# Kernel tuning notes

Measured on AMD Instinct MI355X. Metric: run time of the kernel, lower is better.

Reference implementation:

```python
import jax, jax.numpy as jnp
import numpy as np

R = 4                      # search_range
D = 2 * R + 1              # 9 -> 81 cost channels
FILTERS = [128, 128, 96, 64, 32, 2]


def mish(x):
    return x * jnp.tanh(jax.nn.softplus(x))


def sep_conv(x, dw, pw, b, act):
    # depthwise 3x3 (depth_multiplier=1), then pointwise 1x1, bias after pointwise
    y = jax.lax.conv_general_dilated(
        x, dw, window_strides=(1, 1), padding='SAME',
        dimension_numbers=('NHWC', 'HWIO', 'NHWC'),
        feature_group_count=x.shape[-1])
    y = jax.lax.conv_general_dilated(
        y, pw, window_strides=(1, 1), padding='SAME',
        dimension_numbers=('NHWC', 'HWIO', 'NHWC'))
    if b is not None:
        y = y + b
    return mish(y) if act else y


def cost_volume(prv, nxt):
    B, H, W, C = prv.shape
    pad = jnp.pad(nxt, ((0, 0), (R, R), (R, R), (0, 0)))
    # (2R+1)^2 shifted correlations, mean over channels (matches tf.reduce_mean axis=3)
    costs = [jnp.mean(prv * pad[:, i:i + H, j:j + W, :], axis=3)
             for i in range(D) for j in range(D)]
    return jnp.stack(costs, axis=3)  # [B,H,W,81]


def setup_inputs() -> dict:
    key = jax.random.key(0)
    ks = jax.random.split(key, 40)
    B, H, W, C = 8, 128, 128, 128
    inp = {
        'prv': jax.random.normal(ks[0], (B, H, W, C), jnp.float32),
        'nxt': jax.random.normal(ks[1], (B, H, W, C), jnp.float32),
    }
    in_ch = [D * D + 2 * C] + FILTERS[:-1]  # [337,128,128,96,64,32]
    ki = 2
    for i, (ci, f) in enumerate(zip(in_ch, FILTERS)):
        inp[f'dw{i}'] = jax.random.normal(ks[ki], (3, 3, 1, ci), jnp.float32) * 0.05; ki += 1
        inp[f'pw{i}'] = jax.random.normal(ks[ki], (1, 1, ci, f), jnp.float32) * 0.05; ki += 1
        if i < len(FILTERS) - 1:  # last layer: use_bias=False
            inp[f'b{i}'] = jnp.zeros((f,), jnp.float32)
    return inp


def reference(prv, nxt,
              dw0, pw0, b0, dw1, pw1, b1, dw2, pw2, b2,
              dw3, pw3, b3, dw4, pw4, b4, dw5, pw5):
    cost = cost_volume(prv, nxt)
    x = jnp.concatenate([cost, prv, nxt], axis=-1)
    x = sep_conv(x, dw0, pw0, b0, True)
    x = sep_conv(x, dw1, pw1, b1, True)
    x = sep_conv(x, dw2, pw2, b2, True)
    x = sep_conv(x, dw3, pw3, b3, True)
    x = sep_conv(x, dw4, pw4, b4, True)
    x = sep_conv(x, dw5, pw5, None, False)  # flow head: no bias, no activation
    return x
```

## Files before the change

kernel.cpp:

```cpp
#include <hip/hip_runtime.h>
#include <math.h>

#define BATCH 8
#define HH 128
#define WW 128
#define CC 128
#define RR 4
#define DDIM 9
#define NS 81
#define NSP 96
#define HWPIX (HH*WW)
#define DSLAB 1032

typedef short  short8  __attribute__((ext_vector_type(8)));
typedef float  f32x4   __attribute__((ext_vector_type(4)));

__device__ __forceinline__ short bf16h(float f){
    unsigned u = __float_as_uint(f);
    u += 0x7fffu + ((u >> 16) & 1u);
    return (short)(u >> 16);
}
__device__ __forceinline__ float bf16f(short s){
    return __uint_as_float(((unsigned)(unsigned short)s) << 16);
}
__device__ __forceinline__ float mish_f(float x){
    float xc = fminf(x, 30.f);
    float t = expf(xc);
    float u = t*t + 2.f*t;
    return x * (u / (u + 2.f));
}

__device__ __forceinline__ void gld16(float* lds, const float* g){
    __builtin_amdgcn_global_load_lds(
        (const __attribute__((address_space(1))) unsigned int*)g,
        (__attribute__((address_space(3))) unsigned int*)lds, 16, 0, 0);
}

__device__ __forceinline__ void lds_barrier(){
    __asm volatile("s_waitcnt lgkmcnt(0)\n\ts_barrier" ::: "memory");
}

__global__ void zero_k(float* p, int n){
    int i = blockIdx.x*256 + threadIdx.x;
    if(i < n) p[i] = 0.f;
}

__global__ __launch_bounds__(256,2) void cost_kernel(
    const float* __restrict__ prv, const float* __restrict__ nxt,
    const float* __restrict__ zb, float* __restrict__ cost)
{
    __shared__ float nx[2][576*12];
    const int tid = threadIdx.x;
    const int tx = tid & 15, ty = tid >> 4;
    const int x0 = blockIdx.x*16, y0 = blockIdx.y*16, b = blockIdx.z;

    float acc[NS];
#pragma unroll
    for(int s=0;s<NS;s++) acc[s]=0.f;

    const float* prvp = prv + (((size_t)b*HH + (y0+ty))*WW + (x0+tx))*CC;
    const float* nxb  = nxt + (size_t)b*HH*WW*CC;

    auto stagec = [&](int c0, int pb){
        float* xp = &nx[pb][0];
#pragma unroll
        for(int it=0;it<7;it++){
            int e = it*256 + tid;
            if(e < 1728){
                int px = e/3, q = e - px*3;
                int hy = y0 - RR + px/24, hx = x0 - RR + px%24;
                bool ok = (q < 2) && hy>=0 && hy<HH && hx>=0 && hx<WW;
                const float* gp = ok ? (nxb + ((size_t)hy*WW + hx)*CC + c0 + q*4)
                                     : zb;
                gld16(xp + px*12 + q*4, gp);
            }
        }
    };

    float4 pAr = *(const float4*)(prvp);
    float4 pBr = *(const float4*)(prvp + 4);
    stagec(0, 0);
    int pb = 0;
    for(int c0=0;c0<CC;c0+=8){
        __syncthreads();
        float4 A = pAr, Bv = pBr;
        if(c0+8 < CC){
            pAr = *(const float4*)(prvp + c0 + 8);
            pBr = *(const float4*)(prvp + c0 + 12);
            stagec(c0+8, pb^1);
        }
        const float* xp = &nx[pb][0];
#pragma unroll
        for(int i=0;i<DDIM;i++){
#pragma unroll
            for(int j=0;j<DDIM;j++){
                const float* q = &xp[((ty+i)*24 + (tx+j))*12];
                float4 n0 = *(const float4*)q;
                float4 n1 = *(const float4*)(q+4);
                float s = acc[i*DDIM+j];
                s = fmaf(A.x,n0.x,s);  s = fmaf(A.y,n0.y,s);
                s = fmaf(A.z,n0.z,s);  s = fmaf(A.w,n0.w,s);
                s = fmaf(Bv.x,n1.x,s); s = fmaf(Bv.y,n1.y,s);
                s = fmaf(Bv.z,n1.z,s); s = fmaf(Bv.w,n1.w,s);
                acc[i*DDIM+j] = s;
            }
        }
        pb ^= 1;
    }
    float* op = cost + (((size_t)b*HH + (y0+ty))*WW + (x0+tx))*NSP;
#pragma unroll
    for(int g=0; g<NSP/4; g++){
        float4 v;
        int s = g*4;
        v.x = (s   < NS) ? acc[s  ]*(1.f/128.f) : 0.f;
        v.y = (s+1 < NS) ? acc[s+1]*(1.f/128.f) : 0.f;
        v.z = (s+2 < NS) ? acc[s+2]*(1.f/128.f) : 0.f;
        v.w = (s+3 < NS) ? acc[s+3]*(1.f/128.f) : 0.f;
        *(float4*)(op + s) = v;
    }
}

__global__ void prep_pw(const float* __restrict__ src, short* __restrict__ dh,
                        short* __restrict__ dl, int K, int N, int NP, int total,
                        int remap)
{
    int idx = blockIdx.x*256 + threadIdx.x;
    if(idx >= total) return;
    int j  = idx & 7;
    int n  = (idx>>3) % NP;
    int k8 = (idx>>3) / NP;
    int k  = k8*8 + j;
    if(remap) k = (k < 81) ? k : ((k < 96) ? -1 : k - 15);
    float v = (k>=0 && k<K && n<N) ? src[(size_t)k*N + n] : 0.f;
    short h = bf16h(v);
    dh[idx] = h;
    dl[idx] = bf16h(v - bf16f(h));
}

__global__ void prep_dw(const float* __restrict__ src, float* __restrict__ dst,
                        int K, int K0, int remap, int total)
{
    int idx = blockIdx.x*256 + threadIdx.x;
    if(idx >= total) return;
    int k = idx / K0, c = idx - k*K0;
    int cr = c;
    if(remap) cr = (c < 81) ? c : ((c < 96) ? -1 : c - 15);
    dst[idx] = (cr>=0 && cr<K) ? src[k*K + cr] : 0.f;
}

template<int CINR,int K0,int COUT,int NP,bool BIAS,bool ACT,bool CONCAT>
__global__ __launch_bounds__(256,2) void sep_mfma(
    const float* __restrict__ xin, const float* __restrict__ cost,
    const float* __restrict__ prv, const float* __restrict__ nxt,
    const float* __restrict__ dwp, const short* __restrict__ wh,
    const short* __restrict__ wl, const float* __restrict__ bias,
    const float* __restrict__ zb, float* __restrict__ out)
{
    constexpr int TN = NP/32;
    __shared__ float xs[2][180*36];
    __shared__ short dshh[4*DSLAB];
    __shared__ short dshl[4*DSLAB];
    __shared__ float dwls[2][9*32];

    const int tid = threadIdx.x;
    const int x0 = blockIdx.x*16, y0 = blockIdx.y*8, b = blockIdx.z;
    const int lane = tid & 63;
    const int wv   = tid >> 6;
    const int wm   = wv >> 1, wn = wv & 1;
    const int l15  = lane & 15, quad = lane >> 4;

    f32x4 acc[4][TN];
#pragma unroll
    for(int i=0;i<4;i++)
#pragma unroll
        for(int nt=0;nt<TN;nt++) acc[i][nt] = (f32x4){0.f,0.f,0.f,0.f};

    auto stage = [&](int c0, int pb){
        if(tid < 72)
            gld16(&dwls[pb][(tid>>3)*32 + (tid&7)*4],
                  dwp + (tid>>3)*K0 + c0 + (tid&7)*4);
        const float* src; int str, coff;
        if(CONCAT){
            if(c0 < 96)      { src = cost; str = NSP; coff = c0; }
            else if(c0 < 224){ src = prv;  str = 128; coff = c0-96; }
            else             { src = nxt;  str = 128; coff = c0-224; }
        } else { src = xin; str = CINR; coff = c0; }
        const float* sb = src + (size_t)b*HH*WW*str + coff;
        float* xp = &xs[pb][0];
#pragma unroll
        for(int it=0;it<7;it++){
            int e = it*256 + tid;
            if(e < 1620){
                int hp = e/9, q = e - hp*9;
                int hy = y0-1 + hp/18, hx = x0-1 + hp%18;
                bool ok = (q < 8) && hy>=0 && hy<HH && hx>=0 && hx<WW;
                const float* gp = ok ? (sb + ((size_t)hy*WW + hx)*str + q*4)
                                     : zb;
                gld16(xp + hp*36 + q*4, gp);
            }
        }
    };

    const int c4  = tid & 7;
    const int pxg = tid >> 3;
    const int dpy = pxg >> 2;
    const int dxb = (pxg & 3) * 4;

    stage(0, 0);
    int pb = 0;
    for(int c0=0;c0<K0;c0+=32){
        __syncthreads();
        const int k8 = (c0>>3) + quad;
        short8 Bh[TN], Bl[TN];
#pragma unroll
        for(int nt=0;nt<TN;nt++){
            int n = wn*(NP/2) + nt*16 + l15;
            size_t off = ((size_t)k8*NP + n)*8;
            Bh[nt] = *(const short8*)(wh + off);
            Bl[nt] = *(const short8*)(wl + off);
        }
        if(c0+32 < K0) stage(c0+32, pb^1);
        const float* xp = &xs[pb][0];
        const float* dwc = &dwls[pb][0];
        {
            float4 o[4];
#pragma unroll
            for(int dx=0;dx<4;dx++) o[dx] = make_float4(0.f,0.f,0.f,0.f);
#pragma unroll
            for(int kh=0;kh<3;kh++){
                float4 xw[6];
#pragma unroll
                for(int t=0;t<6;t++)
                    xw[t] = *(const float4*)&xp[((dpy+kh)*18 + dxb + t)*36 + c4*4];
#pragma unroll
                for(int kw=0;kw<3;kw++){
                    float4 w4 = *(const float4*)&dwc[(kh*3+kw)*32 + c4*4];
#pragma unroll
                    for(int dx=0;dx<4;dx++){
                        float4 xv = xw[kw+dx];
                        o[dx].x = fmaf(xv.x,w4.x,o[dx].x);
                        o[dx].y = fmaf(xv.y,w4.y,o[dx].y);
                        o[dx].z = fmaf(xv.z,w4.z,o[dx].z);
                        o[dx].w = fmaf(xv.w,w4.w,o[dx].w);
                    }
                }
            }
            const int wbase = (c4>>1)*DSLAB + (pxg*4)*8 + (c4&1)*4;
#pragma unroll
            for(int dx=0;dx<4;dx++){
                float4 s = o[dx];
                short h0=bf16h(s.x), h1=bf16h(s.y), h2=bf16h(s.z), h3=bf16h(s.w);
                short l0=bf16h(s.x-bf16f(h0)), l1=bf16h(s.y-bf16f(h1));
                short l2=bf16h(s.z-bf16f(h2)), l3=bf16h(s.w-bf16f(h3));
                *(short4*)&dshh[wbase + dx*8] = make_short4(h0,h1,h2,h3);
                *(short4*)&dshl[wbase + dx*8] = make_short4(l0,l1,l2,l3);
            }
        }
        lds_barrier();
#pragma unroll
        for(int i=0;i<4;i++){
            int ab = quad*DSLAB + (wm*64 + i*16 + l15)*8;
            short8 Ah = *(const short8*)&dshh[ab];
            short8 Al = *(const short8*)&dshl[ab];
#pragma unroll
            for(int nt=0;nt<TN;nt++){
                f32x4 c = acc[i][nt];
                c = __builtin_amdgcn_mfma_f32_16x16x32_bf16(Ah,Bh[nt],c,0,0,0);
                c = __builtin_amdgcn_mfma_f32_16x16x32_bf16(Al,Bh[nt],c,0,0,0);
                c = __builtin_amdgcn_mfma_f32_16x16x32_bf16(Ah,Bl[nt],c,0,0,0);
                acc[i][nt] = c;
            }
        }
        lds_barrier();
        pb ^= 1;
    }
#pragma unroll
    for(int i=0;i<4;i++){
        int pxb = wm*64 + i*16 + quad*4;
#pragma unroll
        for(int nt=0;nt<TN;nt++){
            int cout = wn*(NP/2) + nt*16 + l15;
            if(cout < COUT){
                float bv = BIAS ? bias[cout] : 0.f;
#pragma unroll
                for(int r=0;r<4;r++){
                    int p = pxb + r;
                    int y = y0 + (p>>4), x = x0 + (p&15);
                    float v = acc[i][nt][r] + bv;
                    if(ACT) v = mish_f(v);
                    out[(((size_t)b*HH + y)*WW + x)*COUT + cout] = v;
                }
            }
        }
    }
}

extern "C" void kernel_launch(void* const* d_in, const int* in_sizes, int n_in,
                              void* d_out, int out_size, void* d_ws, size_t ws_size,
                              hipStream_t stream)
{
    (void)in_sizes; (void)n_in; (void)out_size;
    const float* prv = (const float*)d_in[0];
    const float* nxt = (const float*)d_in[1];
    const float* dws[6] = {(const float*)d_in[2],(const float*)d_in[5],(const float*)d_in[8],
                           (const float*)d_in[11],(const float*)d_in[14],(const float*)d_in[17]};
    const float* pws[6] = {(const float*)d_in[3],(const float*)d_in[6],(const float*)d_in[9],
                           (const float*)d_in[12],(const float*)d_in[15],(const float*)d_in[18]};
    const float* b0  = (const float*)d_in[4];
    const float* b1  = (const float*)d_in[7];
    const float* b2  = (const float*)d_in[10];
    const float* b3  = (const float*)d_in[13];
    const float* b4  = (const float*)d_in[16];

    const int   Ks[6]   = {337,128,128, 96, 64, 32};
    const int   K0s[6]  = {352,128,128, 96, 64, 32};
    const int   Ns[6]   = {128,128, 96, 64, 32,  2};
    const int   NPs[6]  = {128,128, 96, 64, 32, 32};
    const int   rmp[6]  = {  1,  0,  0,  0,  0,  0};
    size_t offs[6]; size_t E = 0;
    for(int i=0;i<6;i++){ offs[i] = E; E += (size_t)K0s[i]*NPs[i]; }
    size_t dwoffs[6]; size_t Edw = 0;
    for(int i=0;i<6;i++){ dwoffs[i] = Edw; Edw += (size_t)9*K0s[i]; }

    short* Whs = (short*)d_ws;
    short* Wls = Whs + E;
    float* Dwp = (float*)((char*)d_ws + ((E*2*sizeof(short) + 255) & ~(size_t)255));
    float* Zb  = Dwp + Edw;
    size_t wbytes = (((char*)(Zb + 64) - (char*)d_ws) + 255) & ~(size_t)255;

    zero_k<<<1,64,0,stream>>>(Zb, 64);
    for(int i=0;i<6;i++){
        int total = K0s[i]*NPs[i];
        prep_pw<<<(total+255)/256,256,0,stream>>>(pws[i], Whs+offs[i], Wls+offs[i],
                                                  Ks[i], Ns[i], NPs[i], total, rmp[i]);
        int tdw = 9*K0s[i];
        prep_dw<<<(tdw+255)/256,256,0,stream>>>(dws[i], Dwp+dwoffs[i],
                                                Ks[i], K0s[i], rmp[i], tdw);
    }

    const size_t per_batch_floats = (size_t)HWPIX * (NSP + 128 + 128);
    size_t avail = (ws_size > wbytes) ? (ws_size - wbytes) : 0;
    int NB = (int)(avail / (per_batch_floats * sizeof(float)));
    if(NB > BATCH) NB = BATCH;
    if(NB < 1)     NB = 1;
    while(BATCH % NB) NB--;

    float* fbase = (float*)((char*)d_ws + wbytes);
    float* costb = fbase;
    float* bufA  = costb + (size_t)NB*HWPIX*NSP;
    float* bufB  = bufA  + (size_t)NB*HWPIX*128;

    for(int bb=0; bb<BATCH; bb+=NB){
        const float* prv_o = prv + (size_t)bb*HWPIX*CC;
        const float* nxt_o = nxt + (size_t)bb*HWPIX*CC;
        float*       out_o = (float*)d_out + (size_t)bb*HWPIX*2;
        dim3 gc(WW/16, HH/16, NB);
        dim3 gs(WW/16, HH/8,  NB);

        cost_kernel<<<gc,256,0,stream>>>(prv_o, nxt_o, Zb, costb);
        sep_mfma<337,352,128,128,true ,true ,true ><<<gs,256,0,stream>>>(nullptr, costb, prv_o, nxt_o, Dwp+dwoffs[0], Whs+offs[0], Wls+offs[0], b0, Zb, bufA);
        sep_mfma<128,128,128,128,true ,true ,false><<<gs,256,0,stream>>>(bufA, nullptr,nullptr,nullptr, Dwp+dwoffs[1], Whs+offs[1], Wls+offs[1], b1, Zb, bufB);
        sep_mfma<128,128, 96, 96,true ,true ,false><<<gs,256,0,stream>>>(bufB, nullptr,nullptr,nullptr, Dwp+dwoffs[2], Whs+offs[2], Wls+offs[2], b2, Zb, bufA);
        sep_mfma< 96, 96, 64, 64,true ,true ,false><<<gs,256,0,stream>>>(bufA, nullptr,nullptr,nullptr, Dwp+dwoffs[3], Whs+offs[3], Wls+offs[3], b3, Zb, bufB);
        sep_mfma< 64, 64, 32, 32,true ,true ,false><<<gs,256,0,stream>>>(bufB, nullptr,nullptr,nullptr, Dwp+dwoffs[4], Whs+offs[4], Wls+offs[4], b4, Zb, bufA);
        sep_mfma< 32, 32,  2, 32,false,false,false><<<gs,256,0,stream>>>(bufA, nullptr,nullptr,nullptr, Dwp+dwoffs[5], Whs+offs[5], Wls+offs[5], nullptr, Zb, out_o);
    }
}
```

Baseline: 576.9 us.

## Compute two output rows per thread in cost kernel to reuse LDS loads

```diff
diff --git a/kernel.cpp b/kernel.cpp
--- a/kernel.cpp
+++ b/kernel.cpp
@@ -45,78 +45,100 @@
     if(i < n) p[i] = 0.f;
 }
 
-__global__ __launch_bounds__(256,2) void cost_kernel(
+__global__ __launch_bounds__(128,2) void cost_kernel(
     const float* __restrict__ prv, const float* __restrict__ nxt,
     const float* __restrict__ zb, float* __restrict__ cost)
 {
-    __shared__ float nx[2][576*12];
+    __shared__ float nx[2][1152*4];
     const int tid = threadIdx.x;
     const int tx = tid & 15, ty = tid >> 4;
     const int x0 = blockIdx.x*16, y0 = blockIdx.y*16, b = blockIdx.z;
-
-    float acc[NS];
-#pragma unroll
-    for(int s=0;s<NS;s++) acc[s]=0.f;
-
-    const float* prvp = prv + (((size_t)b*HH + (y0+ty))*WW + (x0+tx))*CC;
+    const int yA = y0 + 2*ty;
+
+    float acc0[NS], acc1[NS];
+#pragma unroll
+    for(int s=0;s<NS;s++){ acc0[s]=0.f; acc1[s]=0.f; }
+
+    const float* prvA = prv + (((size_t)b*HH + yA)*WW + (x0+tx))*CC;
+    const float* prvB = prvA + (size_t)WW*CC;
     const float* nxb  = nxt + (size_t)b*HH*WW*CC;
 
     auto stagec = [&](int c0, int pb){
         float* xp = &nx[pb][0];
 #pragma unroll
-        for(int it=0;it<7;it++){
-            int e = it*256 + tid;
-            if(e < 1728){
-                int px = e/3, q = e - px*3;
-                int hy = y0 - RR + px/24, hx = x0 - RR + px%24;
-                bool ok = (q < 2) && hy>=0 && hy<HH && hx>=0 && hx<WW;
-                const float* gp = ok ? (nxb + ((size_t)hy*WW + hx)*CC + c0 + q*4)
-                                     : zb;
-                gld16(xp + px*12 + q*4, gp);
-            }
+        for(int it=0;it<9;it++){
+            int e = it*128 + tid;
+            int q = (e >= 576) ? 1 : 0;
+            int p = e - q*576;
+            int row = p/24, col = p - row*24;
+            int hy = y0 - RR + row, hx = x0 - RR + col;
+            bool ok = hy>=0 && hy<HH && hx>=0 && hx<WW;
+            const float* gp = ok ? (nxb + ((size_t)hy*WW + hx)*CC + c0 + q*4)
+                                 : zb;
+            gld16(xp + e*4, gp);
         }
     };
 
-    float4 pAr = *(const float4*)(prvp);
-    float4 pBr = *(const float4*)(prvp + 4);
+    float4 pA0r = *(const float4*)(prvA);
+    float4 pB0r = *(const float4*)(prvA + 4);
+    float4 pA1r = *(const float4*)(prvB);
+    float4 pB1r = *(const float4*)(prvB + 4);
     stagec(0, 0);
     int pb = 0;
     for(int c0=0;c0<CC;c0+=8){
         __syncthreads();
-        float4 A = pAr, Bv = pBr;
+        float4 A0 = pA0r, B0 = pB0r, A1 = pA1r, B1 = pB1r;
         if(c0+8 < CC){
-            pAr = *(const float4*)(prvp + c0 + 8);
-            pBr = *(const float4*)(prvp + c0 + 12);
+            pA0r = *(const float4*)(prvA + c0 + 8);
+            pB0r = *(const float4*)(prvA + c0 + 12);
+            pA1r = *(const float4*)(prvB + c0 + 8);
+            pB1r = *(const float4*)(prvB + c0 + 12);
             stagec(c0+8, pb^1);
         }
         const float* xp = &nx[pb][0];
 #pragma unroll
-        for(int i=0;i<DDIM;i++){
+        for(int i=0;i<10;i++){
+            const float* rp = xp + (((2*ty + i)*24) + tx)*4;
 #pragma unroll
             for(int j=0;j<DDIM;j++){
-                const float* q = &xp[((ty+i)*24 + (tx+j))*12];
-                float4 n0 = *(const float4*)q;
-                float4 n1 = *(const float4*)(q+4);
-                float s = acc[i*DDIM+j];
-                s = fmaf(A.x,n0.x,s);  s = fmaf(A.y,n0.y,s);
-                s = fmaf(A.z,n0.z,s);  s = fmaf(A.w,n0.w,s);
-                s = fmaf(Bv.x,n1.x,s); s = fmaf(Bv.y,n1.y,s);
-                s = fmaf(Bv.z,n1.z,s); s = fmaf(Bv.w,n1.w,s);
-                acc[i*DDIM+j] = s;
+                float4 n0 = *(const float4*)(rp + j*4);
+                float4 n1 = *(const float4*)(rp + j*4 + 2304);
+                if(i < 9){
+                    float s = acc0[i*DDIM+j];
+                    s = fmaf(A0.x,n0.x,s);  s = fmaf(A0.y,n0.y,s);
+                    s = fmaf(A0.z,n0.z,s);  s = fmaf(A0.w,n0.w,s);
+                    s = fmaf(B0.x,n1.x,s);  s = fmaf(B0.y,n1.y,s);
+                    s = fmaf(B0.z,n1.z,s);  s = fmaf(B0.w,n1.w,s);
+                    acc0[i*DDIM+j] = s;
+                }
+                if(i > 0){
+                    float s = acc1[(i-1)*DDIM+j];
+                    s = fmaf(A1.x,n0.x,s);  s = fmaf(A1.y,n0.y,s);
+                    s = fmaf(A1.z,n0.z,s);  s = fmaf(A1.w,n0.w,s);
+                    s = fmaf(B1.x,n1.x,s);  s = fmaf(B1.y,n1.y,s);
+                    s = fmaf(B1.z,n1.z,s);  s = fmaf(B1.w,n1.w,s);
+                    acc1[(i-1)*DDIM+j] = s;
+                }
             }
         }
         pb ^= 1;
     }
-    float* op = cost + (((size_t)b*HH + (y0+ty))*WW + (x0+tx))*NSP;
+    float* opA = cost + (((size_t)b*HH + yA)*WW + (x0+tx))*NSP;
+    float* opB = opA + (size_t)WW*NSP;
 #pragma unroll
     for(int g=0; g<NSP/4; g++){
-        float4 v;
         int s = g*4;
-        v.x = (s   < NS) ? acc[s  ]*(1.f/128.f) : 0.f;
-        v.y = (s+1 < NS) ? acc[s+1]*(1.f/128.f) : 0.f;
-        v.z = (s+2 < NS) ? acc[s+2]*(1.f/128.f) : 0.f;
-        v.w = (s+3 < NS) ? acc[s+3]*(1.f/128.f) : 0.f;
-        *(float4*)(op + s) = v;
+        float4 v0, v1;
+        v0.x = (s   < NS) ? acc0[s  ]*(1.f/128.f) : 0.f;
+        v0.y = (s+1 < NS) ? acc0[s+1]*(1.f/128.f) : 0.f;
+        v0.z = (s+2 < NS) ? acc0[s+2]*(1.f/128.f) : 0.f;
+        v0.w = (s+3 < NS) ? acc0[s+3]*(1.f/128.f) : 0.f;
+        v1.x = (s   < NS) ? acc1[s  ]*(1.f/128.f) : 0.f;
+        v1.y = (s+1 < NS) ? acc1[s+1]*(1.f/128.f) : 0.f;
+        v1.z = (s+2 < NS) ? acc1[s+2]*(1.f/128.f) : 0.f;
+        v1.w = (s+3 < NS) ? acc1[s+3]*(1.f/128.f) : 0.f;
+        *(float4*)(opA + s) = v0;
+        *(float4*)(opB + s) = v1;
     }
 }
 
@@ -357,7 +379,7 @@
         dim3 gc(WW/16, HH/16, NB);
         dim3 gs(WW/16, HH/8,  NB);
 
-        cost_kernel<<<gc,256,0,stream>>>(prv_o, nxt_o, Zb, costb);
+        cost_kernel<<<gc,128,0,stream>>>(prv_o, nxt_o, Zb, costb);
         sep_mfma<337,352,128,128,true ,true ,true ><<<gs,256,0,stream>>>(nullptr, costb, prv_o, nxt_o, Dwp+dwoffs[0], Whs+offs[0], Wls+offs[0], b0, Zb, bufA);
         sep_mfma<128,128,128,128,true ,true ,false><<<gs,256,0,stream>>>(bufA, nullptr,nullptr,nullptr, Dwp+dwoffs[1], Whs+offs[1], Wls+offs[1], b1, Zb, bufB);
         sep_mfma<128,128, 96, 96,true ,true ,false><<<gs,256,0,stream>>>(bufB, nullptr,nullptr,nullptr, Dwp+dwoffs[2], Whs+offs[2], Wls+offs[2], b2, Zb, bufA);
```

After: 635.1 us. 1.1x slower.
